# Performance work log

Measured on AMD Instinct MI355X. Metric: run time of the kernel, lower is better.

## Reference

```python
import jax, jax.numpy as jnp
import numpy as np

CS = [32, 32, 64, 128, 256, 256, 128, 96, 96]
NC = 19
N0, N1, N2, N3, N4 = 50000, 20000, 8000, 3200, 1300


def build_shapes():
    cs = CS
    def rb(ci, co):
        t = [(27, ci, co), (27, co, co)]
        if ci != co:
            t.append((ci, co))  # 1x1 shortcut conv
        return t
    s = [(27, 4, cs[0]), (27, cs[0], cs[0])]                       # stem
    s += [(8, cs[0], cs[0])] + rb(cs[0], cs[1]) + rb(cs[1], cs[1])  # stage1
    s += [(8, cs[1], cs[1])] + rb(cs[1], cs[2]) + rb(cs[2], cs[2])  # stage2
    s += [(8, cs[2], cs[2])] + rb(cs[2], cs[3]) + rb(cs[3], cs[3])  # stage3
    s += [(8, cs[3], cs[3])] + rb(cs[3], cs[4]) + rb(cs[4], cs[4])  # stage4
    s += [(8, cs[4], cs[5])] + rb(cs[5] + cs[3], cs[5]) + rb(cs[5], cs[5])  # up1
    s += [(8, cs[5], cs[6])] + rb(cs[6] + cs[2], cs[6]) + rb(cs[6], cs[6])  # up2
    s += [(8, cs[6], cs[7])] + rb(cs[7] + cs[1], cs[7]) + rb(cs[7], cs[7])  # up3
    s += [(8, cs[7], cs[8])] + rb(cs[8] + cs[0], cs[8]) + rb(cs[8], cs[8])  # up4
    s += [(cs[8], NC), (NC,), (cs[8], cs[8]), (cs[8],), (cs[8], 128), (128,)]
    return s

P_TOTAL = sum(int(np.prod(sh)) for sh in build_shapes())


def _bn(x):
    # train-mode BatchNorm, gamma=1 beta=0 (set by weight_initialization)
    return (x - x.mean(0)) * jax.lax.rsqrt(jnp.var(x, 0) + 1e-5)


def _spconv(x, nbr, W):
    # sparse conv as gather-GEMM-scatter over K kernel offsets.
    # x: [Nin, Cin], nbr: [Nout, K] row indices into x, W: [K, Cin, Cout]
    acc0 = jnp.zeros((nbr.shape[0], W.shape[-1]), x.dtype)
    def step(acc, kw):
        idx, Wk = kw
        return acc + x[idx] @ Wk, None
    acc, _ = jax.lax.scan(step, acc0, (nbr.T, W))
    return acc


def _spdeconv(x, parent, off, W):
    # transposed ks=2 stride=2 conv: each fine voxel has exactly one coarse
    # parent and one kernel-offset id. out[i] = x[parent[i]] @ W[off[i]]
    y = jnp.einsum('nc,kcd->nkd', x[parent], W)  # [Nf, 8, Cout]
    return jnp.take_along_axis(y, off[:, None, None], axis=1)[:, 0, :]


def _cbr(x, nbr, W):
    return jax.nn.relu(_bn(_spconv(x, nbr, W)))


def _resblock(x, nbr, take, ci, co):
    w1 = take(); w2 = take()
    h = _bn(_spconv(jax.nn.relu(_bn(_spconv(x, nbr, w1))), nbr, w2))
    s = x if ci == co else _bn(x @ take())
    return jax.nn.relu(h + s)


def _forward(x, nbr0, nbr1, nbr2, nbr3, nbr4, d1, d2, d3, d4,
             u1p, u1o, u2p, u2o, u3p, u3o, u4p, u4o, params):
    parts = []
    o = 0
    for sh in build_shapes():
        n = int(np.prod(sh))
        parts.append(params[o:o + n].reshape(sh))
        o += n
    it = iter(parts)
    take = lambda: next(it)
    cs = CS
    x0 = _cbr(x, nbr0, take()); x0 = _cbr(x0, nbr0, take())            # stem
    h = _cbr(x0, d1, take())
    h = _resblock(h, nbr1, take, cs[0], cs[1]); x1 = _resblock(h, nbr1, take, cs[1], cs[1])
    h = _cbr(x1, d2, take())
    h = _resblock(h, nbr2, take, cs[1], cs[2]); x2 = _resblock(h, nbr2, take, cs[2], cs[2])
    h = _cbr(x2, d3, take())
    h = _resblock(h, nbr3, take, cs[2], cs[3]); x3 = _resblock(h, nbr3, take, cs[3], cs[3])
    h = _cbr(x3, d4, take())
    h = _resblock(h, nbr4, take, cs[3], cs[4]); x4 = _resblock(h, nbr4, take, cs[4], cs[4])
    y = jax.nn.relu(_bn(_spdeconv(x4, u1p, u1o, take())))
    y = jnp.concatenate([y, x3], 1)
    y = _resblock(y, nbr3, take, cs[5] + cs[3], cs[5]); y = _resblock(y, nbr3, take, cs[5], cs[5])
    y = jax.nn.relu(_bn(_spdeconv(y, u2p, u2o, take())))
    y = jnp.concatenate([y, x2], 1)
    y = _resblock(y, nbr2, take, cs[6] + cs[2], cs[6]); y = _resblock(y, nbr2, take, cs[6], cs[6])
    y = jax.nn.relu(_bn(_spdeconv(y, u3p, u3o, take())))
    y = jnp.concatenate([y, x1], 1)
    y = _resblock(y, nbr1, take, cs[7] + cs[1], cs[7]); y = _resblock(y, nbr1, take, cs[7], cs[7])
    y = jax.nn.relu(_bn(_spdeconv(y, u4p, u4o, take())))
    y = jnp.concatenate([y, x0], 1)
    y = _resblock(y, nbr0, take, cs[8] + cs[0], cs[8]); y = _resblock(y, nbr0, take, cs[8], cs[8])
    wc = take(); bc = take(); w1 = take(); b1 = take(); w2 = take(); b2 = take()
    out = y @ wc + bc                             # classifier logits [N0, NC]
    feat = jax.nn.relu(y @ w1 + b1) @ w2 + b2     # projection head [N0, 128]
    return out, feat


def setup_inputs() -> dict:
    key = jax.random.key(0)
    ks = jax.random.split(key, 20)
    ri = lambda k, shape, hi: jax.random.randint(k, shape, 0, hi, dtype=jnp.int32)
    return {
        'x': jax.random.normal(ks[0], (N0, 4), jnp.float32),
        'nbr0': ri(ks[1], (N0, 27), N0), 'nbr1': ri(ks[2], (N1, 27), N1),
        'nbr2': ri(ks[3], (N2, 27), N2), 'nbr3': ri(ks[4], (N3, 27), N3),
        'nbr4': ri(ks[5], (N4, 27), N4),
        'd1': ri(ks[6], (N1, 8), N0), 'd2': ri(ks[7], (N2, 8), N1),
        'd3': ri(ks[8], (N3, 8), N2), 'd4': ri(ks[9], (N4, 8), N3),
        'u1p': ri(ks[10], (N3,), N4), 'u1o': ri(ks[11], (N3,), 8),
        'u2p': ri(ks[12], (N2,), N3), 'u2o': ri(ks[13], (N2,), 8),
        'u3p': ri(ks[14], (N1,), N2), 'u3o': ri(ks[15], (N1,), 8),
        'u4p': ri(ks[16], (N0,), N1), 'u4o': ri(ks[17], (N0,), 8),
        'params': jax.random.normal(ks[18], (P_TOTAL,), jnp.float32) * 0.05,
    }


def reference(x, nbr0, nbr1, nbr2, nbr3, nbr4, d1, d2, d3, d4,
              u1p, u1o, u2p, u2o, u3p, u3o, u4p, u4o, params):
    return _forward(x, nbr0, nbr1, nbr2, nbr3, nbr4, d1, d2, d3, d4,
                    u1p, u1o, u2p, u2o, u3p, u3o, u4p, u4o, params)
```

## Files before the change

### kernel.cpp

```cpp
#include <hip/hip_runtime.h>
#include <hip/hip_bf16.h>
#include <stdint.h>

typedef __hip_bfloat16 hbf;
typedef unsigned short u16;
typedef __attribute__((ext_vector_type(8))) short bfrag;
typedef __attribute__((ext_vector_type(4))) float f4;

#define NP0 50000
#define NP1 20000
#define NP2 8000
#define NP3 3200
#define NP4 1300

static inline int cdiv(int a, int b) { return (a + b - 1) / b; }

static __device__ __forceinline__ float u2f(u16 u) { return __uint_as_float(((unsigned)u) << 16); }
static __device__ __forceinline__ u16 f2u(float f) {
  hbf h = __float2bfloat16(f);
  u16 r; __builtin_memcpy(&r, &h, 2); return r;
}
static __device__ __forceinline__ float pload(const void* P, int isbf, size_t i) {
  return isbf ? u2f(((const u16*)P)[i]) : ((const float*)P)[i];
}


__global__ void k_sniff(const void* __restrict__ xraw, int* __restrict__ flagp) {
  __shared__ float smax[256];
  const u16* u = (const u16*)xraw;
  float m = 0.f;
  for (int i = threadIdx.x; i < 2048; i += 256) {
    float v = u2f(u[2 * i]);
    if (isnan(v) || isinf(v)) m = 1e30f; else m = fmaxf(m, fabsf(v));
  }
  smax[threadIdx.x] = m;
  __syncthreads();
  for (int s = 128; s > 0; s >>= 1) {
    if (threadIdx.x < s) smax[threadIdx.x] = fmaxf(smax[threadIdx.x], smax[threadIdx.x + s]);
    __syncthreads();
  }
  if (threadIdx.x == 0) *flagp = (smax[0] < 1e4f) ? 1 : 0;
}

__global__ __launch_bounds__(256) void k_prep_frag(
    const void* __restrict__ P, const int* __restrict__ flagp, u16* __restrict__ W,
    long src, long halfel, int K, int CI, int CO, int CB32, int NT16)
{
  int f = *flagp;
  long total = (long)K * CB32 * NT16 * 64;
  for (long c = (long)blockIdx.x * 256 + threadIdx.x; c < total; c += (long)gridDim.x * 256) {
    int lane = (int)(c & 63); long t = c >> 6;
    int nt = (int)(t % NT16); t /= NT16;
    int cb = (int)(t % CB32); int k = (int)(t / CB32);
    int co = nt * 16 + (lane & 15);
    int cib = cb * 32 + (lane >> 4) * 8;
    u16 hi[8], lo[8];
#pragma unroll
    for (int j = 0; j < 8; ++j) {
      int ci = cib + j; float v = 0.f;
      if (ci < CI && co < CO) v = pload(P, f, src + ((size_t)k * CI + ci) * CO + co);
      u16 h = f2u(v);
      hi[j] = h;
      lo[j] = f2u(v - u2f(h));
    }
    *(bfrag*)(W + c * 8) = *(const bfrag*)hi;
    *(bfrag*)(W + halfel + c * 8) = *(const bfrag*)lo;
  }
}

__global__ void k_prep_bias(const void* __restrict__ P, const int* __restrict__ flagp,
                            float* __restrict__ B, long src, int n)
{
  int f = *flagp;
  int i = blockIdx.x * 256 + threadIdx.x;
  if (i < n) B[i] = pload(P, f, src + i);
}

__global__ void k_pad(const void* __restrict__ xraw, const int* __restrict__ flagp,
                      u16* __restrict__ Xp2, int N)
{
  int f = *flagp; int total = N * 32;
  for (int i = blockIdx.x * 256 + threadIdx.x; i < total; i += gridDim.x * 256) {
    int n = i >> 5, cc = i & 31;
    float v = (cc < 4) ? pload(xraw, f, (size_t)n * 4 + cc) : 0.f;
    u16 h = f2u(v);
    Xp2[(size_t)n * 64 + cc] = h;
    Xp2[(size_t)n * 64 + 32 + cc] = f2u(v - u2f(h));
  }
}

template<int NT>
__global__ __launch_bounds__(256) void k_conv_mfma(
    const u16* __restrict__ X, const int* __restrict__ nbr,
    const u16* __restrict__ Wp, long halfel, float* __restrict__ Y,
    const float* __restrict__ bias, int relu,
    int N, int K, int CB32, int NT16, int CO, int XS, int tlen, int atomic)
{
  const int lane = threadIdx.x & 63;
  const int wv = threadIdx.x >> 6;
  const int rowbase = blockIdx.x * 128 + wv * 32;
  const int ntb = blockIdx.y * NT;
  const int ml = lane & 15;
  const int quad = lane >> 4;
  const int ktot = K * CB32;
  const int t0 = blockIdx.z * tlen;
  const int t1 = (t0 + tlen < ktot) ? (t0 + tlen) : ktot;

  f4 acc[2][NT];
#pragma unroll
  for (int i = 0; i < 2; ++i)
#pragma unroll
    for (int j = 0; j < NT; ++j) acc[i][j] = (f4)(0.f);

  int k = t0 / CB32;
  int cb = t0 - k * CB32;
  int idx[2];
  bool fresh = true;

  for (int t = t0; t < t1; ++t) {
    if (fresh) {
#pragma unroll
      for (int mt = 0; mt < 2; ++mt) {
        int r = rowbase + mt * 16 + ml;
        idx[mt] = (r < N) ? (nbr ? nbr[(size_t)r * K + k] : r) : 0;
      }
      fresh = false;
    }
    const u16* WH = Wp + (size_t)t * NT16 * 512;
    const u16* WL = WH + halfel;
    bfrag bh[NT], bl[NT];
#pragma unroll
    for (int nt = 0; nt < NT; ++nt) {
      size_t o = ((size_t)(ntb + nt) * 64 + lane) * 8;
      bh[nt] = *(const bfrag*)(WH + o);
      bl[nt] = *(const bfrag*)(WL + o);
    }
    bfrag ahi[2], alo[2];
#pragma unroll
    for (int mt = 0; mt < 2; ++mt) {
      const u16* ap = X + (size_t)idx[mt] * (2 * XS) + cb * 32 + quad * 8;
      ahi[mt] = *(const bfrag*)ap;
      alo[mt] = *(const bfrag*)(ap + XS);
    }
#pragma unroll
    for (int mt = 0; mt < 2; ++mt)
#pragma unroll
      for (int nt = 0; nt < NT; ++nt) {
        acc[mt][nt] = __builtin_amdgcn_mfma_f32_16x16x32_bf16(alo[mt], bh[nt], acc[mt][nt], 0, 0, 0);
        acc[mt][nt] = __builtin_amdgcn_mfma_f32_16x16x32_bf16(ahi[mt], bl[nt], acc[mt][nt], 0, 0, 0);
        acc[mt][nt] = __builtin_amdgcn_mfma_f32_16x16x32_bf16(ahi[mt], bh[nt], acc[mt][nt], 0, 0, 0);
      }
    if (++cb == CB32) { cb = 0; ++k; fresh = true; }
  }

#pragma unroll
  for (int mt = 0; mt < 2; ++mt) {
#pragma unroll
    for (int nt = 0; nt < NT; ++nt) {
      int col = (ntb + nt) * 16 + ml;
      if (col >= CO) continue;
      float bvv = bias ? bias[col] : 0.f;
#pragma unroll
      for (int reg = 0; reg < 4; ++reg) {
        int row = rowbase + mt * 16 + quad * 4 + reg;
        if (row < N) {
          if (atomic) {
            atomicAdd(&Y[(size_t)row * CO + col], acc[mt][nt][reg]);
          } else {
            float v = acc[mt][nt][reg] + bvv;
            if (relu) v = fmaxf(v, 0.f);
            Y[(size_t)row * CO + col] = v;
          }
        }
      }
    }
  }
}

__global__ void k_bias_relu(float* __restrict__ Y, const float* __restrict__ bias,
                            int relu, int total, int CO)
{
  int stride = gridDim.x * 256;
  for (int i = blockIdx.x * 256 + threadIdx.x; i < total; i += stride) {
    int c = i % CO;
    float v = Y[i] + (bias ? bias[c] : 0.f);
    if (relu) v = fmaxf(v, 0.f);
    Y[i] = v;
  }
}

__global__ void k_bias_relu_split(const float* __restrict__ Y, const float* __restrict__ bias,
                                  u16* __restrict__ D2, int relu, int N, int CO)
{
  int co4 = CO >> 2;
  int total4 = N * co4;
  int stride = gridDim.x * 256;
  for (int i = blockIdx.x * 256 + threadIdx.x; i < total4; i += stride) {
    int n = i / co4, c = (i - n * co4) * 4;
    float4 v = ((const float4*)Y)[i];
    float vv[4] = {v.x, v.y, v.z, v.w};
    ushort4 h, l;
    u16 hh[4], ll[4];
#pragma unroll
    for (int j = 0; j < 4; ++j) {
      float x = vv[j] + (bias ? bias[c + j] : 0.f);
      if (relu) x = fmaxf(x, 0.f);
      u16 hu = f2u(x);
      hh[j] = hu; ll[j] = f2u(x - u2f(hu));
    }
    h.x = hh[0]; h.y = hh[1]; h.z = hh[2]; h.w = hh[3];
    l.x = ll[0]; l.y = ll[1]; l.z = ll[2]; l.w = ll[3];
    size_t ho = (size_t)n * 2 * CO + c;
    *(ushort4*)(D2 + ho) = h;
    *(ushort4*)(D2 + ho + CO) = l;
  }
}

static void launch_conv(hipStream_t s, int bx, const u16* X, const int* nbr,
                        const u16* W, long halfel, float* Y, const float* bias, int relu,
                        int N, int K, int CB32, int NT16, int CO, int XS)
{
  int NT = (NT16 % 6 == 0) ? 6 : ((NT16 % 4 == 0) ? 4 : 2);
  int ny = NT16 / NT;
  int ktot = K * CB32;
  long blocks = (long)bx * ny;
  int ZS = 1;
  if (ktot > 1) {
    ZS = (int)((1024 + blocks - 1) / blocks);
    if (ZS > ktot) ZS = ktot;
    if (ZS < 1) ZS = 1;
  }
  int tlen = cdiv(ktot, ZS);
  ZS = cdiv(ktot, tlen);
  int atomic = (ZS > 1) ? 1 : 0;
  if (atomic) hipMemsetAsync(Y, 0, (size_t)N * CO * 4, s);
  dim3 g(bx, ny, ZS);
  if (NT == 6)      k_conv_mfma<6><<<g, 256, 0, s>>>(X, nbr, W, halfel, Y, bias, relu, N, K, CB32, NT16, CO, XS, tlen, atomic);
  else if (NT == 4) k_conv_mfma<4><<<g, 256, 0, s>>>(X, nbr, W, halfel, Y, bias, relu, N, K, CB32, NT16, CO, XS, tlen, atomic);
  else              k_conv_mfma<2><<<g, 256, 0, s>>>(X, nbr, W, halfel, Y, bias, relu, N, K, CB32, NT16, CO, XS, tlen, atomic);
  if (atomic && (bias || relu)) {
    int total = N * CO;
    int nb = cdiv(total, 1024); if (nb > 1024) nb = 1024; if (nb < 1) nb = 1;
    k_bias_relu<<<nb, 256, 0, s>>>(Y, bias, relu, total, CO);
  }
}

__global__ __launch_bounds__(256) void k_deconv(
    const u16* __restrict__ X2, const int* __restrict__ par, const int* __restrict__ off,
    const void* __restrict__ P, long wofs, const int* __restrict__ flagp,
    float* __restrict__ Y, int N, int CI, int CO)
{
  int f = *flagp;
  int lane = threadIdx.x & 63, wv = threadIdx.x >> 6;
  int n = blockIdx.y * 4 + wv; if (n >= N) return;
  int co = blockIdx.x * 64 + lane; if (co >= CO) return;
  const u16* xr = X2 + (size_t)par[n] * 2 * CI;
  size_t wbase = wofs + (size_t)off[n] * CI * CO + co;
  float acc = 0.f;
  for (int ci = 0; ci < CI; ci += 4) {
    ushort4 xh = *(const ushort4*)(xr + ci);
    ushort4 xl = *(const ushort4*)(xr + CI + ci);
    acc += (u2f(xh.x) + u2f(xl.x)) * pload(P, f, wbase + (size_t)ci * CO);
    acc += (u2f(xh.y) + u2f(xl.y)) * pload(P, f, wbase + (size_t)(ci + 1) * CO);
    acc += (u2f(xh.z) + u2f(xl.z)) * pload(P, f, wbase + (size_t)(ci + 2) * CO);
    acc += (u2f(xh.w) + u2f(xl.w)) * pload(P, f, wbase + (size_t)(ci + 3) * CO);
  }
  Y[(size_t)n * CO + co] = acc;
}

__global__ __launch_bounds__(256) void k_bn_stats(
    const float* __restrict__ X, float* __restrict__ st, int total, int C)
{
  __shared__ float ssum[384], ssq[384];
  for (int c = threadIdx.x; c < C; c += 256) { ssum[c] = 0.f; ssq[c] = 0.f; }
  __syncthreads();
  int gid = blockIdx.x * 256 + threadIdx.x;
  int total4 = total >> 2;
  int stride = gridDim.x * 256;
  int c0 = (gid * 4) % C;
  float s0 = 0.f, s1 = 0.f, s2 = 0.f, s3 = 0.f;
  float q0 = 0.f, q1 = 0.f, q2 = 0.f, q3 = 0.f;
  for (int i = gid; i < total4; i += stride) {
    float4 v = ((const float4*)X)[i];
    s0 += v.x; q0 += v.x * v.x;
    s1 += v.y; q1 += v.y * v.y;
    s2 += v.z; q2 += v.z * v.z;
    s3 += v.w; q3 += v.w * v.w;
  }
  atomicAdd(&ssum[c0], s0);     atomicAdd(&ssq[c0], q0);
  atomicAdd(&ssum[c0 + 1], s1); atomicAdd(&ssq[c0 + 1], q1);
  atomicAdd(&ssum[c0 + 2], s2); atomicAdd(&ssq[c0 + 2], q2);
  atomicAdd(&ssum[c0 + 3], s3); atomicAdd(&ssq[c0 + 3], q3);
  __syncthreads();
  for (int c = threadIdx.x; c < C; c += 256) {
    atomicAdd(&st[c], ssum[c]); atomicAdd(&st[384 + c], ssq[c]);
  }
}

__global__ __launch_bounds__(256) void k_bn_apply(
    const float* __restrict__ X, const float* __restrict__ st, const u16* __restrict__ add2,
    u16* __restrict__ Y2, int relu, int total, int C, float invN)
{
  __shared__ float mean[384], rsig[384];
  for (int c = threadIdx.x; c < C; c += 256) {
    float mm = st[c] * invN;
    float vv = st[384 + c] * invN - mm * mm;
    mean[c] = mm; rsig[c] = rsqrtf(vv + 1e-5f);
  }
  __syncthreads();
  int gid = blockIdx.x * 256 + threadIdx.x;
  int total4 = total >> 2;
  int stride = gridDim.x * 256;
  int C4 = C >> 2;
  int c0 = (gid % C4) * 4;
  int n = gid / C4;
  int dn = stride / C4;
  float m0 = mean[c0], m1 = mean[c0 + 1], m2 = mean[c0 + 2], m3 = mean[c0 + 3];
  float r0 = rsig[c0], r1 = rsig[c0 + 1], r2 = rsig[c0 + 2], r3 = rsig[c0 + 3];
  for (int i = gid; i < total4; i += stride, n += dn) {
    float4 v = ((const float4*)X)[i];
    float w0 = (v.x - m0) * r0, w1 = (v.y - m1) * r1;
    float w2 = (v.z - m2) * r2, w3 = (v.w - m3) * r3;
    size_t ho = (size_t)n * 2 * C + c0;
    if (add2) {
      ushort4 ah = *(const ushort4*)(add2 + ho);
      ushort4 al = *(const ushort4*)(add2 + ho + C);
      w0 += u2f(ah.x) + u2f(al.x); w1 += u2f(ah.y) + u2f(al.y);
      w2 += u2f(ah.z) + u2f(al.z); w3 += u2f(ah.w) + u2f(al.w);
    }
    if (relu) {
      w0 = fmaxf(w0, 0.f); w1 = fmaxf(w1, 0.f);
      w2 = fmaxf(w2, 0.f); w3 = fmaxf(w3, 0.f);
    }
    u16 h0 = f2u(w0), h1 = f2u(w1), h2 = f2u(w2), h3 = f2u(w3);
    ushort4 hh; hh.x = h0; hh.y = h1; hh.z = h2; hh.w = h3;
    ushort4 ll;
    ll.x = f2u(w0 - u2f(h0)); ll.y = f2u(w1 - u2f(h1));
    ll.z = f2u(w2 - u2f(h2)); ll.w = f2u(w3 - u2f(h3));
    *(ushort4*)(Y2 + ho) = hh;
    *(ushort4*)(Y2 + ho + C) = ll;
  }
}

__global__ void k_copycols(const u16* __restrict__ S2, u16* __restrict__ D2,
                           int N, int Cs, int Cd, int off)
{
  int csq = Cs >> 2;
  int total4 = N * csq;
  int stride = gridDim.x * 256;
  for (int i = blockIdx.x * 256 + threadIdx.x; i < total4; i += stride) {
    int n = i / csq, cc = (i - n * csq) * 4;
    size_t so = (size_t)n * 2 * Cs + cc;
    size_t dd = (size_t)n * 2 * Cd + off + cc;
    *(ushort4*)(D2 + dd) = *(const ushort4*)(S2 + so);
    *(ushort4*)(D2 + dd + Cd) = *(const ushort4*)(S2 + so + Cs);
  }
}

__global__ void k_store_dyn(const float* __restrict__ S, void* __restrict__ D,
                            const int* __restrict__ flagp, size_t eofs, int n)
{
  int f = *flagp;
  int n4 = n >> 2;
  int stride = gridDim.x * 256;
  for (int i = blockIdx.x * 256 + threadIdx.x; i < n4; i += stride) {
    float4 v = ((const float4*)S)[i];
    if (f) {
      ushort4 u;
      u.x = f2u(v.x); u.y = f2u(v.y); u.z = f2u(v.z); u.w = f2u(v.w);
      *(ushort4*)((u16*)D + eofs + (size_t)i * 4) = u;
    } else {
      *(float4*)((float*)D + eofs + (size_t)i * 4) = v;
    }
  }
}


extern "C" void kernel_launch(void* const* d_in, const int* in_sizes, int n_in,
                              void* d_out, int out_size, void* d_ws, size_t ws_size,
                              hipStream_t stream)
{
  const void* xraw = d_in[0];
  const int* nbr0 = (const int*)d_in[1];
  const int* nbr1 = (const int*)d_in[2];
  const int* nbr2 = (const int*)d_in[3];
  const int* nbr3 = (const int*)d_in[4];
  const int* nbr4 = (const int*)d_in[5];
  const int* d1 = (const int*)d_in[6];
  const int* d2 = (const int*)d_in[7];
  const int* d3 = (const int*)d_in[8];
  const int* d4 = (const int*)d_in[9];
  const int* u1p = (const int*)d_in[10]; const int* u1o = (const int*)d_in[11];
  const int* u2p = (const int*)d_in[12]; const int* u2o = (const int*)d_in[13];
  const int* u3p = (const int*)d_in[14]; const int* u3o = (const int*)d_in[15];
  const int* u4p = (const int*)d_in[16]; const int* u4o = (const int*)d_in[17];
  const void* params = d_in[18];
  (void)in_sizes; (void)n_in;

  char* base = (char*)d_ws; size_t off = 0;
  auto ab = [&](size_t bytes) -> void* { void* p = base + off; off += (bytes + 63) & ~(size_t)63; return p; };
  int* flagp = (int*)ab(64);
  float* st = (float*)ab((size_t)64 * 768 * 4);
  u16* Wst = (u16*)ab((size_t)5400000 * 2);
  float* Bstf = (float*)ab((size_t)512 * 4);
  u16* x0 = (u16*)ab((size_t)NP0 * 32 * 4);
  u16* x1 = (u16*)ab((size_t)NP1 * 32 * 4);
  u16* x2 = (u16*)ab((size_t)NP2 * 64 * 4);
  u16* x3 = (u16*)ab((size_t)NP3 * 128 * 4);
  u16* x4 = (u16*)ab((size_t)NP4 * 256 * 4);
  float* U  = (float*)ab((size_t)NP0 * 96 * 4);
  float* A  = (float*)ab((size_t)NP0 * 96 * 4);
  float* B  = (float*)ab((size_t)NP0 * 128 * 4);
  u16* Xp = (u16*)B;
  if (off > ws_size) { hipMemsetAsync(d_out, 0, (size_t)out_size * 2, stream); return; }

  long po = 0;
  int bnc = 0;

  auto prepF = [&](int K, int CI, int CO, int CB32, int NT16) -> long {
    long chunks = (long)K * CB32 * NT16 * 64;
    long halfel = chunks * 8;
    int nb = (int)((chunks + 255) / 256); if (nb > 4096) nb = 4096; if (nb < 1) nb = 1;
    k_prep_frag<<<nb, 256, 0, stream>>>(params, flagp, Wst, po, halfel, K, CI, CO, CB32, NT16);
    po += (long)K * CI * CO;
    return halfel;
  };
  auto convop = [&](const u16* X2, const int* nb_, int K, int CI, int CO, float* Y, int N, int XS) {
    int CB32 = cdiv(CI, 32), NT16 = cdiv(CO, 16);
    long halfel = prepF(K, CI, CO, CB32, NT16);
    launch_conv(stream, cdiv(N, 128), X2, nb_, Wst, halfel, Y, nullptr, 0, N, K, CB32, NT16, CO, XS);
  };
  auto linop = [&](const u16* X2, int CI, int CO, float* Y, int N, bool bias, int relu, u16* osplit) {
    int CB32 = cdiv(CI, 32), NT16 = cdiv(CO, 16);
    long halfel = prepF(1, CI, CO, CB32, NT16);
    const float* bp = nullptr;
    if (bias) {
      k_prep_bias<<<cdiv(CO, 256), 256, 0, stream>>>(params, flagp, Bstf, po, CO);
      po += CO; bp = Bstf;
    }
    if (osplit) {
      launch_conv(stream, cdiv(N, 128), X2, nullptr, Wst, halfel, Y, nullptr, 0, N, 1, CB32, NT16, CO, CI);
      int nb = cdiv((N * CO) >> 2, 1024); if (nb > 1024) nb = 1024; if (nb < 1) nb = 1;
      k_bias_relu_split<<<nb, 256, 0, stream>>>(Y, bp, osplit, relu, N, CO);
    } else {
      launch_conv(stream, cdiv(N, 128), X2, nullptr, Wst, halfel, Y, bp, relu, N, 1, CB32, NT16, CO, CI);
    }
  };
  auto deconvop = [&](const u16* X2, const int* par, const int* ofv, int CI, int CO, float* Y, int N) {
    long wofs = po; po += (long)8 * CI * CO;
    dim3 g(cdiv(CO, 64), cdiv(N, 4));
    k_deconv<<<g, 256, 0, stream>>>(X2, par, ofv, params, wofs, flagp, Y, N, CI, CO);
  };
  auto bnop = [&](const float* X, int N, int C, const u16* add2, int relu, u16* out2) {
    float* slot = st + (size_t)(bnc++) * 768;
    int total = N * C;
    int total4 = total >> 2;
    int nb1 = cdiv(total4, 4096); if (nb1 > 504) nb1 = 504; if (nb1 < 3) nb1 = 3;
    nb1 = ((nb1 + 2) / 3) * 3;
    k_bn_stats<<<nb1, 256, 0, stream>>>(X, slot, total, C);
    int nb2 = cdiv(total4, 2048); if (nb2 > 510) nb2 = 510; if (nb2 < 3) nb2 = 3;
    nb2 = ((nb2 + 2) / 3) * 3;
    k_bn_apply<<<nb2, 256, 0, stream>>>(X, slot, add2, out2, relu, total, C, 1.0f / (float)N);
  };
  auto copyop = [&](const u16* S2, u16* D2, int N, int Cs, int Cd, int o2) {
    int total4 = (N * Cs) >> 2;
    int nb3 = cdiv(total4, 1024); if (nb3 > 1024) nb3 = 1024; if (nb3 < 1) nb3 = 1;
    k_copycols<<<nb3, 256, 0, stream>>>(S2, D2, N, Cs, Cd, o2);
  };
  auto storeop = [&](const float* S, size_t eo, int n) {
    int nb4 = cdiv(n >> 2, 1024); if (nb4 > 1024) nb4 = 1024; if (nb4 < 1) nb4 = 1;
    k_store_dyn<<<nb4, 256, 0, stream>>>(S, d_out, flagp, eo, n);
  };
  auto resblock = [&](const int* nb, int N, int CI, int CO,
                      float* H, float* t1, float* t2, float* OUT) {
    convop((const u16*)H, nb, 27, CI, CO, t1, N, CI);
    bnop(t1, N, CO, nullptr, 1, (u16*)t2);
    convop((const u16*)t2, nb, 27, CO, CO, t1, N, CO);
    if (CI == CO) {
      bnop(t1, N, CO, (const u16*)H, 1, (u16*)OUT);
    } else {
      linop((const u16*)H, CI, CO, t2, N, false, 0, nullptr);
      bnop(t2, N, CO, nullptr, 0, (u16*)OUT);
      bnop(t1, N, CO, (const u16*)OUT, 1, (u16*)OUT);
    }
  };

  k_sniff<<<1, 256, 0, stream>>>(xraw, flagp);
  hipMemsetAsync(st, 0, (size_t)64 * 768 * 4, stream);
  k_pad<<<1024, 256, 0, stream>>>(xraw, flagp, Xp, NP0);

  convop(Xp, nbr0, 27, 4, 32, U, NP0, 32);
  bnop(U, NP0, 32, nullptr, 1, (u16*)A);
  convop((const u16*)A, nbr0, 27, 32, 32, U, NP0, 32);
  bnop(U, NP0, 32, nullptr, 1, x0);
  convop(x0, d1, 8, 32, 32, A, NP1, 32); bnop(A, NP1, 32, nullptr, 1, (u16*)U);
  resblock(nbr1, NP1, 32, 32, U, A, B, U);
  resblock(nbr1, NP1, 32, 32, U, A, B, (float*)x1);
  convop(x1, d2, 8, 32, 32, A, NP2, 32); bnop(A, NP2, 32, nullptr, 1, (u16*)U);
  resblock(nbr2, NP2, 32, 64, U, A, B, U);
  resblock(nbr2, NP2, 64, 64, U, A, B, (float*)x2);
  convop(x2, d3, 8, 64, 64, A, NP3, 64); bnop(A, NP3, 64, nullptr, 1, (u16*)U);
  resblock(nbr3, NP3, 64, 128, U, A, B, U);
  resblock(nbr3, NP3, 128, 128, U, A, B, (float*)x3);
  convop(x3, d4, 8, 128, 128, A, NP4, 128); bnop(A, NP4, 128, nullptr, 1, (u16*)U);
  resblock(nbr4, NP4, 128, 256, U, A, B, U);
  resblock(nbr4, NP4, 256, 256, U, A, B, (float*)x4);
  deconvop(x4, u1p, u1o, 256, 256, A, NP3); bnop(A, NP3, 256, nullptr, 1, (u16*)U);
  copyop((u16*)U, (u16*)B, NP3, 256, 384, 0); copyop(x3, (u16*)B, NP3, 128, 384, 256);
  resblock(nbr3, NP3, 384, 256, B, A, U, B);
  resblock(nbr3, NP3, 256, 256, B, A, U, U);
  deconvop((const u16*)U, u2p, u2o, 256, 128, A, NP2); bnop(A, NP2, 128, nullptr, 1, (u16*)U);
  copyop((u16*)U, (u16*)B, NP2, 128, 192, 0); copyop(x2, (u16*)B, NP2, 64, 192, 128);
  resblock(nbr2, NP2, 192, 128, B, A, U, B);
  resblock(nbr2, NP2, 128, 128, B, A, U, U);
  deconvop((const u16*)U, u3p, u3o, 128, 96, A, NP1); bnop(A, NP1, 96, nullptr, 1, (u16*)U);
  copyop((u16*)U, (u16*)B, NP1, 96, 128, 0); copyop(x1, (u16*)B, NP1, 32, 128, 96);
  resblock(nbr1, NP1, 128, 96, B, A, U, B);
  resblock(nbr1, NP1, 96, 96, B, A, U, U);
  deconvop((const u16*)U, u4p, u4o, 96, 96, A, NP0); bnop(A, NP0, 96, nullptr, 1, (u16*)U);
  copyop((u16*)U, (u16*)B, NP0, 96, 128, 0); copyop(x0, (u16*)B, NP0, 32, 128, 96);
  resblock(nbr0, NP0, 128, 96, B, A, U, B);
  resblock(nbr0, NP0, 96, 96, B, A, U, U);
  float* x0f = (float*)x0;
  linop((const u16*)U, 96, 19, x0f, NP0, true, 0, nullptr);
  linop((const u16*)U, 96, 96, B, NP0, true, 1, (u16*)A);
  linop((const u16*)A, 96, 128, B, NP0, true, 0, nullptr);
  storeop(x0f, 0, NP0 * 19);
  storeop(B, (size_t)NP0 * 19, NP0 * 128);
}
```

Baseline: 4.590 ms.

## Skip low-part weight MFMA when params are bf16 and prefetch neighbor indices

The conv kernel now reads the input dtype flag and, when weights are bf16 (whose low split part is zero), skips loading the low weight fragments and the third MFMA pass. Neighbor indices for the next kernel offset are prefetched one iteration early to hide gather-index latency. The split-K target block count also rises from 1024 to 1536, which adds more atomic partial sums. For fp32 params the low-part pass is still run, so results stay the same, but the extra branch may add register pressure.

```diff
diff --git a/kernel.cpp b/kernel.cpp
--- a/kernel.cpp
+++ b/kernel.cpp
@@ -93,9 +93,10 @@
 __global__ __launch_bounds__(256) void k_conv_mfma(
     const u16* __restrict__ X, const int* __restrict__ nbr,
     const u16* __restrict__ Wp, long halfel, float* __restrict__ Y,
-    const float* __restrict__ bias, int relu,
+    const float* __restrict__ bias, int relu, const int* __restrict__ flagp,
     int N, int K, int CB32, int NT16, int CO, int XS, int tlen, int atomic)
 {
+  const int f = *flagp;
   const int lane = threadIdx.x & 63;
   const int wv = threadIdx.x >> 6;
   const int rowbase = blockIdx.x * 128 + wv * 32;
@@ -115,25 +116,19 @@
   int k = t0 / CB32;
   int cb = t0 - k * CB32;
   int idx[2];
-  bool fresh = true;
+#pragma unroll
+  for (int mt = 0; mt < 2; ++mt) {
+    int r = rowbase + mt * 16 + ml;
+    idx[mt] = (r < N) ? (nbr ? nbr[(size_t)r * K + k] : r) : 0;
+  }
 
   for (int t = t0; t < t1; ++t) {
-    if (fresh) {
-#pragma unroll
-      for (int mt = 0; mt < 2; ++mt) {
-        int r = rowbase + mt * 16 + ml;
-        idx[mt] = (r < N) ? (nbr ? nbr[(size_t)r * K + k] : r) : 0;
-      }
-      fresh = false;
-    }
     const u16* WH = Wp + (size_t)t * NT16 * 512;
-    const u16* WL = WH + halfel;
-    bfrag bh[NT], bl[NT];
+    bfrag bb[NT];
 #pragma unroll
     for (int nt = 0; nt < NT; ++nt) {
       size_t o = ((size_t)(ntb + nt) * 64 + lane) * 8;
-      bh[nt] = *(const bfrag*)(WH + o);
-      bl[nt] = *(const bfrag*)(WL + o);
+      bb[nt] = *(const bfrag*)(WH + o);
     }
     bfrag ahi[2], alo[2];
 #pragma unroll
@@ -142,15 +137,35 @@
       ahi[mt] = *(const bfrag*)ap;
       alo[mt] = *(const bfrag*)(ap + XS);
     }
+    int idxn[2] = {idx[0], idx[1]};
+    if (cb == CB32 - 1 && t + 1 < t1 && nbr) {
+#pragma unroll
+      for (int mt = 0; mt < 2; ++mt) {
+        int r = rowbase + mt * 16 + ml;
+        idxn[mt] = (r < N) ? nbr[(size_t)r * K + (k + 1)] : 0;
+      }
+    }
 #pragma unroll
     for (int mt = 0; mt < 2; ++mt)
 #pragma unroll
       for (int nt = 0; nt < NT; ++nt) {
-        acc[mt][nt] = __builtin_amdgcn_mfma_f32_16x16x32_bf16(alo[mt], bh[nt], acc[mt][nt], 0, 0, 0);
-        acc[mt][nt] = __builtin_amdgcn_mfma_f32_16x16x32_bf16(ahi[mt], bl[nt], acc[mt][nt], 0, 0, 0);
-        acc[mt][nt] = __builtin_amdgcn_mfma_f32_16x16x32_bf16(ahi[mt], bh[nt], acc[mt][nt], 0, 0, 0);
+        acc[mt][nt] = __builtin_amdgcn_mfma_f32_16x16x32_bf16(alo[mt], bb[nt], acc[mt][nt], 0, 0, 0);
+        acc[mt][nt] = __builtin_amdgcn_mfma_f32_16x16x32_bf16(ahi[mt], bb[nt], acc[mt][nt], 0, 0, 0);
       }
-    if (++cb == CB32) { cb = 0; ++k; fresh = true; }
+    if (!f) {
+      const u16* WL = WH + halfel;
+#pragma unroll
+      for (int nt = 0; nt < NT; ++nt) {
+        size_t o = ((size_t)(ntb + nt) * 64 + lane) * 8;
+        bb[nt] = *(const bfrag*)(WL + o);
+      }
+#pragma unroll
+      for (int mt = 0; mt < 2; ++mt)
+#pragma unroll
+        for (int nt = 0; nt < NT; ++nt)
+          acc[mt][nt] = __builtin_amdgcn_mfma_f32_16x16x32_bf16(ahi[mt], bb[nt], acc[mt][nt], 0, 0, 0);
+    }
+    if (++cb == CB32) { cb = 0; ++k; idx[0] = idxn[0]; idx[1] = idxn[1]; }
   }
 
 #pragma unroll
@@ -218,7 +233,7 @@
 
 static void launch_conv(hipStream_t s, int bx, const u16* X, const int* nbr,
                         const u16* W, long halfel, float* Y, const float* bias, int relu,
-                        int N, int K, int CB32, int NT16, int CO, int XS)
+                        const int* flagp, int N, int K, int CB32, int NT16, int CO, int XS)
 {
   int NT = (NT16 % 6 == 0) ? 6 : ((NT16 % 4 == 0) ? 4 : 2);
   int ny = NT16 / NT;
@@ -226,7 +241,7 @@
   long blocks = (long)bx * ny;
   int ZS = 1;
   if (ktot > 1) {
-    ZS = (int)((1024 + blocks - 1) / blocks);
+    ZS = (int)((1536 + blocks - 1) / blocks);
     if (ZS > ktot) ZS = ktot;
     if (ZS < 1) ZS = 1;
   }
@@ -235,9 +250,9 @@
   int atomic = (ZS > 1) ? 1 : 0;
   if (atomic) hipMemsetAsync(Y, 0, (size_t)N * CO * 4, s);
   dim3 g(bx, ny, ZS);
-  if (NT == 6)      k_conv_mfma<6><<<g, 256, 0, s>>>(X, nbr, W, halfel, Y, bias, relu, N, K, CB32, NT16, CO, XS, tlen, atomic);
-  else if (NT == 4) k_conv_mfma<4><<<g, 256, 0, s>>>(X, nbr, W, halfel, Y, bias, relu, N, K, CB32, NT16, CO, XS, tlen, atomic);
-  else              k_conv_mfma<2><<<g, 256, 0, s>>>(X, nbr, W, halfel, Y, bias, relu, N, K, CB32, NT16, CO, XS, tlen, atomic);
+  if (NT == 6)      k_conv_mfma<6><<<g, 256, 0, s>>>(X, nbr, W, halfel, Y, bias, relu, flagp, N, K, CB32, NT16, CO, XS, tlen, atomic);
+  else if (NT == 4) k_conv_mfma<4><<<g, 256, 0, s>>>(X, nbr, W, halfel, Y, bias, relu, flagp, N, K, CB32, NT16, CO, XS, tlen, atomic);
+  else              k_conv_mfma<2><<<g, 256, 0, s>>>(X, nbr, W, halfel, Y, bias, relu, flagp, N, K, CB32, NT16, CO, XS, tlen, atomic);
   if (atomic && (bias || relu)) {
     int total = N * CO;
     int nb = cdiv(total, 1024); if (nb > 1024) nb = 1024; if (nb < 1) nb = 1;
@@ -428,7 +443,7 @@
   auto convop = [&](const u16* X2, const int* nb_, int K, int CI, int CO, float* Y, int N, int XS) {
     int CB32 = cdiv(CI, 32), NT16 = cdiv(CO, 16);
     long halfel = prepF(K, CI, CO, CB32, NT16);
-    launch_conv(stream, cdiv(N, 128), X2, nb_, Wst, halfel, Y, nullptr, 0, N, K, CB32, NT16, CO, XS);
+    launch_conv(stream, cdiv(N, 128), X2, nb_, Wst, halfel, Y, nullptr, 0, flagp, N, K, CB32, NT16, CO, XS);
   };
   auto linop = [&](const u16* X2, int CI, int CO, float* Y, int N, bool bias, int relu, u16* osplit) {
     int CB32 = cdiv(CI, 32), NT16 = cdiv(CO, 16);
@@ -439,11 +454,11 @@
       po += CO; bp = Bstf;
     }
     if (osplit) {
-      launch_conv(stream, cdiv(N, 128), X2, nullptr, Wst, halfel, Y, nullptr, 0, N, 1, CB32, NT16, CO, CI);
+      launch_conv(stream, cdiv(N, 128), X2, nullptr, Wst, halfel, Y, nullptr, 0, flagp, N, 1, CB32, NT16, CO, CI);
       int nb = cdiv((N * CO) >> 2, 1024); if (nb > 1024) nb = 1024; if (nb < 1) nb = 1;
       k_bias_relu_split<<<nb, 256, 0, stream>>>(Y, bp, osplit, relu, N, CO);
     } else {
-      launch_conv(stream, cdiv(N, 128), X2, nullptr, Wst, halfel, Y, bp, relu, N, 1, CB32, NT16, CO, CI);
+      launch_conv(stream, cdiv(N, 128), X2, nullptr, Wst, halfel, Y, bp, relu, flagp, N, 1, CB32, NT16, CO, CI);
     }
   };
   auto deconvop = [&](const u16* X2, const int* par, const int* ofv, int CI, int CO, float* Y, int N) {
```

Result: slower. 5.039 ms (+9.8%).
